# Kernel tuning notes

Hardware: AMD Instinct MI355X
Metric: run time of the kernel (lower is better)

The kernel has to match this reference:

```python
import jax, jax.numpy as jnp
import numpy as np

H, DH, DIM, BNECK, NK, COND = 8, 64, 256, 128, 32, 256


def _ln(x):
    m = x.mean(-1, keepdims=True)
    v = ((x - m) ** 2).mean(-1, keepdims=True)
    return (x - m) * jax.lax.rsqrt(v + 1e-5)


def _mlp(x, w1, b1, w2, b2):
    return jax.nn.gelu(x @ w1 + b1) @ w2 + b2


def _radial(d, w):
    # Bessel-type radial basis sin(n*d)/d projected to heads; limit n as d->0
    n = jnp.arange(1, NK + 1, dtype=d.dtype)
    safe = jnp.maximum(d, 1e-6)[..., None]
    basis = jnp.where(d[..., None] > 1e-6, jnp.sin(d[..., None] * n) / safe, n)
    return jnp.einsum('ijk,kh->hij', basis, w)


def _kernel(x, qk_w):
    # DotProductKernel with softmax=False, scale=1.0
    b, n, _ = x.shape
    qk = (x @ qk_w).reshape(b, n, 2, H, DH).transpose(0, 3, 2, 1, 4)  # b h two n d
    q, k = qk[:, :, 0], qk[:, :, 1]
    return jnp.einsum('bhid,bhjd->bhij', q, k)


def reference(u, lat, lat_diff, lon_diff, scalar_cond, adaLN_w, adaLN_b, to_v_w, to_x_in_w, to_x_w1, to_x_b1, to_x_w2, to_x_b2, to_y_in_w, to_y_w1, to_y_b1, to_y_w2, to_y_b2, kx_qk_w, ky_qk_w, rx_w, ry_w, merge_w, merge_b, ffn_w1, ffn_b1, ffn_w2, ffn_b2):
    b, nlat, nlon, c = u.shape
    mod = (scalar_cond @ adaLN_w + adaLN_b)[:, None, None]  # (b,1,1,6c)
    sh_msa, sc_msa, g_msa, sh_mlp, sc_mlp, g_mlp = jnp.split(mod, 6, axis=-1)
    u_skip = u
    um = _ln(u) * (1 + sc_msa) + sh_msa  # modulate_fused
    lw = jnp.cos(lat)
    lw = lw / lw.mean()
    # PoolingReducer over lat (weighted) -> (b, nlon, bneck)
    u_x = _mlp(jnp.einsum('bilc,cd,i->bld', um, to_x_in_w, lw) / nlat,
               to_x_w1, to_x_b1, to_x_w2, to_x_b2)
    # PoolingReducer over lon -> (b, nlat, bneck)
    u_y = _mlp((um @ to_y_in_w).mean(axis=2), to_y_w1, to_y_b1, to_y_w2, to_y_b2)
    k_x = jax.nn.softmax(_kernel(u_x, kx_qk_w) * _radial(lon_diff, rx_w)[None], axis=-1)
    k_y = jax.nn.softmax(_kernel(u_y, ky_qk_w) * _radial(lat_diff, ry_w)[None], axis=-1)
    v = (um @ to_v_w).reshape(b, nlat, nlon, H, DH).transpose(0, 3, 1, 2, 4)  # b h i l c
    u_phi = jnp.einsum('bhij,bhjmc->bhimc', k_y, v)
    u_phi = jnp.einsum('bhlm,bhimc->bhilc', k_x, u_phi)
    u_phi = u_phi.transpose(0, 2, 3, 1, 4)  # b i l h c
    mu = u_phi.mean(-1, keepdims=True)
    var = ((u_phi - mu) ** 2).mean(-1, keepdims=True)
    gn = ((u_phi - mu) * jax.lax.rsqrt(var + 1e-6)).reshape(b, nlat, nlon, H * DH)
    u1 = u_skip + g_msa * (gn @ merge_w + merge_b)  # bias_dropout_add_scale (inference)
    u2 = _ln(u1) * (1 + sc_mlp) + sh_mlp
    return u1 + g_mlp * _mlp(u2, ffn_w1, ffn_b1, ffn_w2, ffn_b2)


def setup_inputs():
    key = jax.random.key(0)
    ks = jax.random.split(key, 20)
    b, nlat, nlon = 4, 128, 256
    dim, h, dh, bn, cond = DIM, H, DH, BNECK, COND
    f = jnp.float32
    u = jax.random.normal(ks[0], (b, nlat, nlon, dim), f)
    lat = jnp.linspace(-np.pi / 2 + 0.01, np.pi / 2 - 0.01, nlat).astype(f)
    lat_diff = jnp.abs(lat[:, None] - lat[None, :])
    lon = (jnp.arange(nlon) * (2 * np.pi / nlon)).astype(f)
    d = jnp.abs(lon[:, None] - lon[None, :])
    lon_diff = jnp.minimum(d, 2 * np.pi - d)
    scalar_cond = jax.random.normal(ks[1], (b, cond), f)

    def w(k, shape, s=0.02):
        return jax.random.normal(k, shape, f) * s

    return dict(
        u=u, lat=lat, lat_diff=lat_diff, lon_diff=lon_diff, scalar_cond=scalar_cond,
        adaLN_w=w(ks[2], (cond, 6 * dim)), adaLN_b=w(ks[3], (6 * dim,)),
        to_v_w=w(ks[4], (dim, h * dh)),
        to_x_in_w=w(ks[5], (dim, dim)), to_x_w1=w(ks[6], (dim, dim)), to_x_b1=jnp.zeros((dim,), f),
        to_x_w2=w(ks[7], (dim, bn)), to_x_b2=jnp.zeros((bn,), f),
        to_y_in_w=w(ks[8], (dim, dim)), to_y_w1=w(ks[9], (dim, dim)), to_y_b1=jnp.zeros((dim,), f),
        to_y_w2=w(ks[10], (dim, bn)), to_y_b2=jnp.zeros((bn,), f),
        kx_qk_w=w(ks[11], (bn, 2 * h * dh)), ky_qk_w=w(ks[12], (bn, 2 * h * dh)),
        rx_w=w(ks[13], (NK, h), 0.1), ry_w=w(ks[14], (NK, h), 0.1),
        merge_w=w(ks[15], (h * dh, dim)), merge_b=jnp.zeros((dim,), f),
        ffn_w1=w(ks[16], (dim, 4 * dim)), ffn_b1=jnp.zeros((4 * dim,), f),
        ffn_w2=w(ks[17], (4 * dim, dim)), ffn_b2=jnp.zeros((dim,), f))
```

## Files before the change

kernel.cpp:

```cpp
#include <hip/hip_runtime.h>
#include <hip/hip_bf16.h>
#include <math.h>


#define B_ 4
#define NLAT 128
#define NLON 256
#define NTOK (B_*NLAT*NLON)
#define SLOT_ELE ((size_t)16777216)

typedef __hip_bfloat16 bf16;
typedef unsigned short u16;
typedef __attribute__((ext_vector_type(8))) short short8;
typedef __attribute__((ext_vector_type(4))) float f32x4;

__device__ __forceinline__ float b2f(bf16 x){ return __bfloat162float(x); }
__device__ __forceinline__ bf16  f2b(float x){ return __float2bfloat16(x); }
__device__ __forceinline__ u16 f2bits(float x){
  bf16 h = __float2bfloat16(x); return *(u16*)&h;
}
__device__ __forceinline__ float bits2f(u16 u){
  union { unsigned int i; float f; } v; v.i = ((unsigned int)u) << 16; return v.f;
}
__device__ __forceinline__ float gelu_f(float x){
  float x3 = x*x*x;
  return 0.5f*x*(1.0f + tanhf(0.7978845608028654f*(x + 0.044715f*x3)));
}
__device__ __forceinline__ float gelu_fast(float x){
  float t = 0.7978845608028654f*(x + 0.044715f*x*x*x);
  float e = __builtin_amdgcn_exp2f(t * 2.8853900817779268f);
  return x - x*__builtin_amdgcn_rcpf(e + 1.0f);
}
__device__ __forceinline__ float ldin(const void* p, size_t i, int flag){
  return flag ? b2f(((const bf16*)p)[i]) : ((const float*)p)[i];
}
__device__ __forceinline__ short4 pack4(float a, float b, float c, float d){
  short4 r; r.x = (short)f2bits(a); r.y = (short)f2bits(b);
  r.z = (short)f2bits(c); r.w = (short)f2bits(d); return r;
}
__device__ __forceinline__ short8 pack8(float a, float b, float c, float d,
                                        float e, float f, float g, float h){
  short8 r;
  r[0]=(short)f2bits(a); r[1]=(short)f2bits(b); r[2]=(short)f2bits(c); r[3]=(short)f2bits(d);
  r[4]=(short)f2bits(e); r[5]=(short)f2bits(f); r[6]=(short)f2bits(g); r[7]=(short)f2bits(h);
  return r;
}
__device__ __forceinline__ void stage16(const u16* g, u16* l){
  __builtin_amdgcn_global_load_lds(
      (const __attribute__((address_space(1))) void*)g,
      (__attribute__((address_space(3))) void*)l, 16, 0, 0);
}

__global__ void k_detect(const void* lon_diff, int* flag){
  const float c = 0.02454369260617026f;
  float asF = ((const float*)lon_diff)[1];
  float asB = b2f(((const bf16*)lon_diff)[1]);
  float ef = fabsf(asF - c), eb = fabsf(asB - c);
  if (!isfinite(ef)) ef = 1e30f;
  *flag = (eb < ef) ? 1 : 0;
}

struct CvtTab {
  const void* src[27];
  float* dst[27];
  int cum[28];
};
__global__ __launch_bounds__(256) void k_cvtall(CvtTab t, const int* __restrict__ flag,
                                                int total){
  int f = *flag;
  for (int i = blockIdx.x*256 + threadIdx.x; i < total; i += gridDim.x*256){
    int s = 0;
    while (i >= t.cum[s+1]) ++s;
    int off = i - t.cum[s];
    t.dst[s][off] = ldin(t.src[s], off, f);
  }
}

__global__ __launch_bounds__(256) void k_wprep(const float* __restrict__ W,
                                               u16* __restrict__ wf,
                                               int KS, int ldn, int total){
  int gid = blockIdx.x*256 + threadIdx.x;
  if (gid >= total) return;
  int j = gid & 7; int lane = (gid >> 3) & 63; int rest = gid >> 9;
  int ks = rest % KS; int nt = rest / KS;
  int k = ks*32 + (lane >> 4)*8 + j;
  int n = nt*16 + (lane & 15);
  wf[gid] = f2bits(W[(size_t)k*ldn + n]);
}

__global__ __launch_bounds__(256) void k_wprep2(const float* __restrict__ W,
                                                u16* __restrict__ wf){
  int gid = blockIdx.x*256 + threadIdx.x;
  int j = gid & 7; int lane = (gid >> 3) & 63; int rest = gid >> 9;
  int nt = rest & 15; int ksAll = rest >> 4;
  int k = ksAll*32 + (lane >> 4)*8 + j;
  int n = nt*16 + (lane & 15);
  wf[gid] = f2bits(W[(size_t)k*256 + n]);
}

__global__ __launch_bounds__(256) void k_wtrans(const float* __restrict__ W,
                                                u16* __restrict__ WT, int K, int N){
  int gid = blockIdx.x*256 + threadIdx.x;
  if (gid >= K*N) return;
  int k = gid % K, n = gid / K;
  WT[(size_t)n*K + k] = f2bits(W[(size_t)k*N + n]);
}

__global__ __launch_bounds__(256) void k_mod(const float* __restrict__ sc,
                                             const float* __restrict__ w,
                                             const float* __restrict__ bias,
                                             float* __restrict__ mod){
  int gid = blockIdx.x*256 + threadIdx.x;
  int s = gid / 1536, j = gid % 1536;
  float acc = bias[j];
  for (int c = 0; c < 256; ++c) acc += sc[s*256+c] * w[c*1536+j];
  mod[gid] = acc;
}

__global__ __launch_bounds__(128) void k_lw(const float* __restrict__ lat,
                                            float* __restrict__ lw){
  __shared__ float red[128];
  int i = threadIdx.x;
  float cv = cosf(lat[i]);
  red[i] = cv; __syncthreads();
  for (int s = 64; s > 0; s >>= 1){ if (i < s) red[i] += red[i+s]; __syncthreads(); }
  float mean = red[0] * (1.0f/128.0f);
  lw[i] = cv / mean;
}

__global__ __launch_bounds__(256) void k_um2(const void* __restrict__ u,
                                             const float* __restrict__ mod,
                                             u16* __restrict__ um,
                                             const int* __restrict__ flag){
  __shared__ u16 tile[64][264];
  __shared__ float r1[64][4], r2[64][4], mv[64], rs[64];
  __shared__ float ssh[256], ssc[256];
  int f = *flag; int tid = threadIdx.x;
  int t0 = blockIdx.x*64; int b = t0 >> 15;
  ssh[tid] = mod[b*1536 + tid];
  ssc[tid] = mod[b*1536 + 256 + tid];
  for (int it = 0; it < 16; ++it){
    int idx = it*256 + tid;
    int tok = idx >> 6, c4 = idx & 63;
    short4 v4;
    if (f){
      v4 = *(const short4*)((const bf16*)u + ((size_t)(t0+tok))*256 + c4*4);
    } else {
      float4 fv = ((const float4*)u)[((size_t)(t0+tok))*64 + c4];
      v4 = pack4(fv.x, fv.y, fv.z, fv.w);
    }
    *(short4*)&tile[tok][c4*4] = v4;
  }
  __syncthreads();
  {
    int tok = tid >> 2, part = tid & 3;
    float s1 = 0.f, s2 = 0.f;
    for (int c4 = 0; c4 < 16; ++c4){
      short4 v4 = *(const short4*)&tile[tok][part*64 + c4*4];
      float a = bits2f((u16)v4.x), bb = bits2f((u16)v4.y),
            c = bits2f((u16)v4.z), d = bits2f((u16)v4.w);
      s1 += a+bb+c+d; s2 += a*a+bb*bb+c*c+d*d;
    }
    r1[tok][part] = s1; r2[tok][part] = s2;
  }
  __syncthreads();
  if ((tid & 3) == 0){
    int tok = tid >> 2;
    float a1 = r1[tok][0]+r1[tok][1]+r1[tok][2]+r1[tok][3];
    float a2 = r2[tok][0]+r2[tok][1]+r2[tok][2]+r2[tok][3];
    float mean = a1*(1.0f/256.0f);
    float var = a2*(1.0f/256.0f) - mean*mean;
    mv[tok] = mean; rs[tok] = rsqrtf(var + 1e-5f);
  }
  __syncthreads();
  for (int it = 0; it < 16; ++it){
    int idx = it*256 + tid;
    int tok = idx >> 6, c4 = idx & 63;
    float mean = mv[tok], rstd = rs[tok];
    short4 v4 = *(const short4*)&tile[tok][c4*4];
    float y[4]; u16 raw[4] = {(u16)v4.x,(u16)v4.y,(u16)v4.z,(u16)v4.w};
    #pragma unroll
    for (int p = 0; p < 4; ++p){
      int c = c4*4 + p;
      y[p] = (bits2f(raw[p]) - mean)*rstd*(1.0f + ssc[c]) + ssh[c];
    }
    *(short4*)(um + ((size_t)(t0+tok))*256 + c4*4) = pack4(y[0],y[1],y[2],y[3]);
  }
}

__global__ __launch_bounds__(256) void k_redx(const u16* __restrict__ um,
                                              const float* __restrict__ lw,
                                              float* __restrict__ redx){
  __shared__ float lws[128];
  int tid = threadIdx.x;
  if (tid < 128) lws[tid] = lw[tid];
  __syncthreads();
  int gid = blockIdx.x*256 + tid;
  int c = gid & 255; int l = (gid >> 8) & 255; int b = gid >> 16;
  float acc = 0.0f;
  for (int i = 0; i < 128; ++i)
    acc += bits2f(um[(((size_t)(b*128 + i)*256 + l)*256) + c]) * lws[i];
  redx[gid] = acc * (1.0f/128.0f);
}

__global__ __launch_bounds__(256) void k_redy(const u16* __restrict__ um,
                                              float* __restrict__ redy){
  int gid = blockIdx.x*256 + threadIdx.x;
  int c = gid & 255; int i = (gid >> 8) & 127; int b = gid >> 15;
  float acc = 0.0f;
  for (int l = 0; l < 256; ++l)
    acc += bits2f(um[(((size_t)(b*128 + i)*256 + l)*256) + c]);
  redy[gid] = acc * (1.0f/256.0f);
}

__global__ __launch_bounds__(256) void gemm_row2(
    const float* __restrict__ Ax, const float* __restrict__ Wx,
    const float* __restrict__ bx, float* __restrict__ Cx, int Kx, int Nx,
    const float* __restrict__ Ay, const float* __restrict__ Wy,
    const float* __restrict__ by, float* __restrict__ Cy, int Ky, int Ny,
    int nbx, int act){
  __shared__ float As[256];
  int bid = blockIdx.x; int tid = threadIdx.x;
  const float* A; const float* W; const float* bias; float* C; int K, N, r;
  if (bid < nbx){ A=Ax; W=Wx; bias=bx; C=Cx; K=Kx; N=Nx; r=bid; }
  else          { A=Ay; W=Wy; bias=by; C=Cy; K=Ky; N=Ny; r=bid-nbx; }
  for (int k = tid; k < K; k += 256) As[k] = A[(size_t)r*K + k];
  __syncthreads();
  for (int n = tid; n < N; n += 256){
    float a0=0.f, a1=0.f, a2=0.f, a3=0.f;
    for (int k = 0; k < K; k += 4){
      a0 += As[k+0]*W[(size_t)(k+0)*N + n];
      a1 += As[k+1]*W[(size_t)(k+1)*N + n];
      a2 += As[k+2]*W[(size_t)(k+2)*N + n];
      a3 += As[k+3]*W[(size_t)(k+3)*N + n];
    }
    float acc = (a0+a1)+(a2+a3) + (bias ? bias[n] : 0.0f);
    if (act == 1) acc = gelu_f(acc);
    C[(size_t)r*N + n] = acc;
  }
}

__global__ __launch_bounds__(256) void k_radial(const float* __restrict__ d,
                                                const float* __restrict__ w,
                                                float* __restrict__ rad, int n){
  int gid = blockIdx.x*256 + threadIdx.x;
  int nn = n*n;
  int h = gid / nn; int rem = gid % nn;
  float dv = d[rem];
  float safe = fmaxf(dv, 1e-6f);
  float acc = 0.0f;
  for (int k = 0; k < 32; ++k){
    float nk = (float)(k+1);
    float basis = (dv > 1e-6f) ? (sinf(dv*nk)/safe) : nk;
    acc += basis * w[k*8 + h];
  }
  rad[gid] = acc;
}

__global__ __launch_bounds__(256) void k_qkT(const float* __restrict__ qk,
                                             float* __restrict__ kT, int n){
  int gid = blockIdx.x*256 + threadIdx.x;
  int j = gid % n; int rest = gid / n;
  int d = rest & 63; int bh = rest >> 6;
  int b = bh >> 3, h = bh & 7;
  kT[gid] = qk[((size_t)(b*n + j))*1024 + 512 + h*64 + d];
}

__global__ __launch_bounds__(256) void k_attn2(const float* __restrict__ qk,
                                               const float* __restrict__ kT,
                                               const float* __restrict__ rad,
                                               u16* __restrict__ kout, int n){
  extern __shared__ float sm[];
  float* qs = sm; float* red = sm + 64;
  int j = threadIdx.x;
  int bid = blockIdx.x; int i = bid % n; int h = (bid / n) & 7; int b = bid / (n*8);
  if (j < 64) qs[j] = qk[((size_t)(b*n + i))*1024 + h*64 + j];
  __syncthreads();
  const float* kcol = kT + ((size_t)((b*8 + h)*64))*n + j;
  float dot = 0.0f;
  #pragma unroll 8
  for (int d0 = 0; d0 < 64; ++d0) dot += qs[d0]*kcol[(size_t)d0*n];
  float s = dot * rad[((size_t)(h*n + i))*n + j];
  float m = s;
  #pragma unroll
  for (int off = 32; off; off >>= 1) m = fmaxf(m, __shfl_xor(m, off));
  int wv = j >> 6, nw = n >> 6;
  if ((j & 63) == 0) red[wv] = m;
  __syncthreads();
  m = red[0];
  for (int w = 1; w < nw; ++w) m = fmaxf(m, red[w]);
  float e = __builtin_amdgcn_exp2f((s - m)*1.44269504088896f);
  float t = e;
  #pragma unroll
  for (int off = 32; off; off >>= 1) t += __shfl_xor(t, off);
  if ((j & 63) == 0) red[4 + wv] = t;
  __syncthreads();
  t = 0.0f;
  for (int w = 0; w < nw; ++w) t += red[4 + w];
  kout[(size_t)bid*n + j] = f2bits(e / t);
}

__global__ __launch_bounds__(256, 2) void k_v3(const u16* __restrict__ um,
                                               const u16* __restrict__ WvT,
                                               u16* __restrict__ vA,
                                               int b0, size_t bstr){
  __shared__ __align__(16) u16 T[512][72];
  int tid = threadIdx.x;
  int wave = tid>>6, lane = tid&63, quad = lane>>4, l15 = lane&15;
  int bid = blockIdx.x;
  int b = b0 + (bid >> 9);
  int rem = bid & 511;
  int m = rem & 255, jt = rem >> 8;
  const u16* umb = um + ((size_t)b*32768)*256;
  f32x4 acc[8][4];
  #pragma unroll
  for (int mt = 0; mt < 8; ++mt)
    #pragma unroll
    for (int nt = 0; nt < 4; ++nt) acc[mt][nt] = (f32x4){0.f,0.f,0.f,0.f};
  for (int ks = 0; ks < 8; ++ks){
    short8 bfr[4];
    #pragma unroll
    for (int nt = 0; nt < 4; ++nt){
      int j = jt*64 + nt*16 + l15;
      bfr[nt] = *(const short8*)(umb + ((size_t)j*256 + m)*256 + ks*32 + quad*8);
    }
    #pragma unroll
    for (int mt = 0; mt < 8; ++mt){
      short8 a = *(const short8*)(WvT + (size_t)((wave*8+mt)*16 + l15)*256 + ks*32 + quad*8);
      #pragma unroll
      for (int nt = 0; nt < 4; ++nt)
        acc[mt][nt] = __builtin_amdgcn_mfma_f32_16x16x32_bf16(a, bfr[nt], acc[mt][nt], 0, 0, 0);
    }
  }
  #pragma unroll
  for (int mt = 0; mt < 8; ++mt){
    int hc0 = (wave*8+mt)*16 + quad*4;
    #pragma unroll
    for (int nt = 0; nt < 4; ++nt){
      int jp = nt*16 + l15;
      T[hc0+0][jp] = f2bits(acc[mt][nt][0]);
      T[hc0+1][jp] = f2bits(acc[mt][nt][1]);
      T[hc0+2][jp] = f2bits(acc[mt][nt][2]);
      T[hc0+3][jp] = f2bits(acc[mt][nt][3]);
    }
  }
  __syncthreads();
  u16* vAb = vA + (size_t)(b - b0)*bstr;
  for (int it = 0; it < 16; ++it){
    int idx = it*256 + tid;
    int g = idx & 7, hc = idx >> 3;
    short8 v8 = *(const short8*)&T[hc][g*8];
    int h = hc >> 6, c = hc & 63;
    *(short8*)(vAb + (size_t)h*2097152 + ((size_t)c*256 + m)*128 + jt*64 + g*8) = v8;
  }
}

__global__ __launch_bounds__(256) void k_phi1c(const u16* __restrict__ kyb,
                                               const u16* __restrict__ vA,
                                               u16* __restrict__ phi,
                                               int b0, size_t bstr){
  int tid = threadIdx.x;
  int wave = tid>>6, lane = tid&63, quad = lane>>4, l15 = lane&15;
  int bid = blockIdx.x;
  int b = b0 + (bid >> 9);
  int rem = bid & 511; int mblk = rem & 63, h = rem >> 6;
  int m0 = mblk*256;
  const u16* vAh = vA + (size_t)(b - b0)*bstr + (size_t)h*2097152;
  u16* phib = phi + (size_t)(b - b0)*bstr;
  const u16* kyh = kyb + (size_t)(b*8+h)*16384;
  f32x4 acc[4][8];
  #pragma unroll
  for (int mt = 0; mt < 4; ++mt)
    #pragma unroll
    for (int nt = 0; nt < 8; ++nt) acc[mt][nt] = (f32x4){0.f,0.f,0.f,0.f};
  for (int ks = 0; ks < 4; ++ks){
    short8 bfr[8];
    #pragma unroll
    for (int nt = 0; nt < 8; ++nt)
      bfr[nt] = *(const short8*)(kyh + (size_t)(nt*16 + l15)*128 + ks*32 + quad*8);
    #pragma unroll
    for (int mt = 0; mt < 4; ++mt){
      int cm = m0 + (wave*4+mt)*16 + l15;
      short8 a = *(const short8*)(vAh + (size_t)cm*128 + ks*32 + quad*8);
      #pragma unroll
      for (int nt = 0; nt < 8; ++nt)
        acc[mt][nt] = __builtin_amdgcn_mfma_f32_16x16x32_bf16(a, bfr[nt], acc[mt][nt], 0, 0, 0);
    }
  }
  #pragma unroll
  for (int mt = 0; mt < 4; ++mt){
    int cmr = m0 + (wave*4+mt)*16 + quad*4;
    #pragma unroll
    for (int nt = 0; nt < 8; ++nt){
      int i = nt*16 + l15;
      *(short4*)(phib + (size_t)h*2097152 + (size_t)i*16384 + cmr)
        = pack4(acc[mt][nt][0], acc[mt][nt][1], acc[mt][nt][2], acc[mt][nt][3]);
    }
  }
}

__global__ __launch_bounds__(256) void k_phi2b(const u16* __restrict__ kxb,
                                               const u16* __restrict__ phi,
                                               u16* __restrict__ OUTt,
                                               int b0, size_t bstr){
  int tid = threadIdx.x;
  int wave = tid>>6, lane = tid&63, quad = lane>>4, l15 = lane&15;
  int bid = blockIdx.x;
  int b = b0 + (bid >> 9);
  int rem = bid & 511; int mblk = rem & 63, h = rem >> 6;
  int m0 = mblk*128;
  int mhalf = (wave&1)*4, nhalf = (wave>>1)*8;
  const u16* ph = phi + (size_t)(b - b0)*bstr + (size_t)h*2097152;
  u16* OUTb = OUTt + (size_t)(b - b0)*bstr;
  const u16* kxh = kxb + (size_t)(b*8+h)*65536;
  f32x4 acc[4][8];
  #pragma unroll
  for (int mt = 0; mt < 4; ++mt)
    #pragma unroll
    for (int nt = 0; nt < 8; ++nt) acc[mt][nt] = (f32x4){0.f,0.f,0.f,0.f};
  for (int ks = 0; ks < 8; ++ks){
    short8 bfr[8];
    #pragma unroll
    for (int nt = 0; nt < 8; ++nt)
      bfr[nt] = *(const short8*)(kxh + (size_t)((nhalf+nt)*16 + l15)*256 + ks*32 + quad*8);
    #pragma unroll
    for (int mt = 0; mt < 4; ++mt){
      int m2 = m0 + (mhalf+mt)*16 + l15;
      short8 a = *(const short8*)(ph + (size_t)m2*256 + ks*32 + quad*8);
      #pragma unroll
      for (int nt = 0; nt < 8; ++nt)
        acc[mt][nt] = __builtin_amdgcn_mfma_f32_16x16x32_bf16(a, bfr[nt], acc[mt][nt], 0, 0, 0);
    }
  }
  #pragma unroll
  for (int mt = 0; mt < 4; ++mt){
    int m2r = m0 + (mhalf+mt)*16 + quad*4;
    #pragma unroll
    for (int nt = 0; nt < 8; ++nt){
      int l = (nhalf+nt)*16 + l15;
      *(short4*)(OUTb + (size_t)h*2097152 + (size_t)l*8192 + m2r)
        = pack4(acc[mt][nt][0], acc[mt][nt][1], acc[mt][nt][2], acc[mt][nt][3]);
    }
  }
}

__global__ __launch_bounds__(256) void k_gnb(const u16* __restrict__ OUTt,
                                             u16* __restrict__ gn,
                                             int b0, size_t bstr){
  int tid = threadIdx.x;
  int bid = blockIdx.x;
  int bi = bid >> 11;
  int rem = bid & 2047; int l = rem & 255, h = rem >> 8;
  int i = tid >> 1, half = tid & 1;
  const u16* src = OUTt + (size_t)bi*bstr + (size_t)h*2097152 + (size_t)l*8192 + i*64 + half*32;
  float v[32]; float s1 = 0.f, s2 = 0.f;
  #pragma unroll
  for (int c4 = 0; c4 < 8; ++c4){
    short4 v4 = *(const short4*)(src + c4*4);
    v[c4*4+0] = bits2f((u16)v4.x); v[c4*4+1] = bits2f((u16)v4.y);
    v[c4*4+2] = bits2f((u16)v4.z); v[c4*4+3] = bits2f((u16)v4.w);
  }
  #pragma unroll
  for (int c = 0; c < 32; ++c){ s1 += v[c]; s2 += v[c]*v[c]; }
  s1 += __shfl_xor(s1, 1); s2 += __shfl_xor(s2, 1);
  float mean = s1*(1.0f/64.0f);
  float var = s2*(1.0f/64.0f) - mean*mean;
  float rstd = rsqrtf(var + 1e-6f);
  u16* dst = gn + (size_t)bi*bstr + ((size_t)(i*256 + l))*512 + h*64 + half*32;
  #pragma unroll
  for (int c4 = 0; c4 < 8; ++c4)
    *(short4*)(dst + c4*4) = pack4((v[c4*4+0]-mean)*rstd, (v[c4*4+1]-mean)*rstd,
                                   (v[c4*4+2]-mean)*rstd, (v[c4*4+3]-mean)*rstd);
}

__global__ __launch_bounds__(256) void k_mergeb(const u16* __restrict__ gn,
                                                const u16* __restrict__ WmT,
                                                const float* __restrict__ biasm,
                                                const float* __restrict__ mod,
                                                const void* __restrict__ u,
                                                void* __restrict__ outv,
                                                const int* __restrict__ flag,
                                                int b0, size_t bstr){
  __shared__ float smg[256], sbb[256];
  int f = *flag;
  int tid = threadIdx.x;
  int bid = blockIdx.x;
  int b = b0 + (bid >> 8);
  int t0 = (bid & 255)*128;
  smg[tid] = mod[b*1536 + 512 + tid];
  sbb[tid] = biasm[tid];
  __syncthreads();
  int wave = tid>>6, lane = tid&63, quad = lane>>4, l15 = lane&15;
  const u16* gnb = gn + (size_t)(b - b0)*bstr;
  int nt0 = wave*2;
  f32x4 acc[16][2];
  #pragma unroll
  for (int mt = 0; mt < 16; ++mt){ acc[mt][0] = (f32x4){0.f,0.f,0.f,0.f}; acc[mt][1] = (f32x4){0.f,0.f,0.f,0.f}; }
  for (int ks = 0; ks < 16; ++ks){
    short8 bfr[2];
    #pragma unroll
    for (int nti = 0; nti < 2; ++nti){
      int tok = t0 + (nt0+nti)*16 + l15;
      bfr[nti] = *(const short8*)(gnb + (size_t)tok*512 + ks*32 + quad*8);
    }
    #pragma unroll
    for (int mt = 0; mt < 16; ++mt){
      short8 a = *(const short8*)(WmT + (size_t)(mt*16 + l15)*512 + ks*32 + quad*8);
      #pragma unroll
      for (int nti = 0; nti < 2; ++nti)
        acc[mt][nti] = __builtin_amdgcn_mfma_f32_16x16x32_bf16(a, bfr[nti], acc[mt][nti], 0, 0, 0);
    }
  }
  #pragma unroll
  for (int mt = 0; mt < 16; ++mt){
    int d0 = mt*16 + quad*4;
    #pragma unroll
    for (int nti = 0; nti < 2; ++nti){
      int tok = t0 + (nt0+nti)*16 + l15;
      size_t o = ((size_t)b*32768 + tok)*256 + d0;
      float r0,r1,r2,r3;
      if (f){
        short4 rv = *(const short4*)((const bf16*)u + o);
        r0 = bits2f((u16)rv.x); r1 = bits2f((u16)rv.y); r2 = bits2f((u16)rv.z); r3 = bits2f((u16)rv.w);
      } else {
        float4 rv = *(const float4*)((const float*)u + o);
        r0 = rv.x; r1 = rv.y; r2 = rv.z; r3 = rv.w;
      }
      float y0 = r0 + smg[d0+0]*(acc[mt][nti][0] + sbb[d0+0]);
      float y1 = r1 + smg[d0+1]*(acc[mt][nti][1] + sbb[d0+1]);
      float y2 = r2 + smg[d0+2]*(acc[mt][nti][2] + sbb[d0+2]);
      float y3 = r3 + smg[d0+3]*(acc[mt][nti][3] + sbb[d0+3]);
      if (f) *(short4*)((bf16*)outv + o) = pack4(y0,y1,y2,y3);
      else   *(float4*)((float*)outv + o) = (float4){y0,y1,y2,y3};
    }
  }
}

__global__ __launch_bounds__(256, 2) void k_ffn4(
    const float* __restrict__ mod,
    const u16* __restrict__ w1f,
    const float* __restrict__ b1c,
    const u16* __restrict__ w2f,
    const float* __restrict__ b2c,
    void* __restrict__ outv,
    const int* __restrict__ flag){
  __shared__ __align__(16) u16 wbuf[2][16384];
  __shared__ __align__(16) u16 hs[64][40];
  int f = *flag;
  int tid = threadIdx.x;
  int wave = tid>>6, lane = tid&63, quad = lane>>4, l15 = lane&15;
  int mrow = wave*16;
  int t0 = blockIdx.x*64;
  int bb = t0 >> 15;
  const float* modp = mod + bb*1536;
  size_t rowbase = ((size_t)(t0 + mrow + l15))*256;

  {
    #pragma unroll
    for (int i = 0; i < 8; ++i){
      int seg = wave*8 + i;
      const u16* src = (seg < 16)
          ? (w1f + (size_t)seg*512 + lane*8)
          : (w2f + (size_t)(seg-16)*512 + lane*8);
      stage16(src, &wbuf[0][seg*512]);
    }
  }

  short8 afr[8];
  float s1 = 0.f, s2 = 0.f;
  #pragma unroll
  for (int ks = 0; ks < 8; ++ks){
    int c0 = ks*32 + quad*8;
    float v0,v1,v2,v3,v4,v5,v6,v7;
    if (f){
      short8 r = *(const short8*)((const bf16*)outv + rowbase + c0);
      afr[ks] = r;
      v0 = bits2f((u16)r[0]); v1 = bits2f((u16)r[1]); v2 = bits2f((u16)r[2]); v3 = bits2f((u16)r[3]);
      v4 = bits2f((u16)r[4]); v5 = bits2f((u16)r[5]); v6 = bits2f((u16)r[6]); v7 = bits2f((u16)r[7]);
    } else {
      float4 fa = *(const float4*)((const float*)outv + rowbase + c0);
      float4 fb = *(const float4*)((const float*)outv + rowbase + c0 + 4);
      v0=fa.x; v1=fa.y; v2=fa.z; v3=fa.w; v4=fb.x; v5=fb.y; v6=fb.z; v7=fb.w;
      afr[ks] = pack8(v0,v1,v2,v3,v4,v5,v6,v7);
    }
    s1 += v0+v1+v2+v3+v4+v5+v6+v7;
    s2 += v0*v0+v1*v1+v2*v2+v3*v3+v4*v4+v5*v5+v6*v6+v7*v7;
  }
  s1 += __shfl_xor(s1, 16); s1 += __shfl_xor(s1, 32);
  s2 += __shfl_xor(s2, 16); s2 += __shfl_xor(s2, 32);
  float mean = s1*(1.0f/256.0f);
  float var = s2*(1.0f/256.0f) - mean*mean;
  float rstd = rsqrtf(var + 1e-5f);
  #pragma unroll
  for (int ks = 0; ks < 8; ++ks){
    int c0 = ks*32 + quad*8;
    float4 sh0 = *(const float4*)&modp[768 + c0];
    float4 sh1 = *(const float4*)&modp[768 + c0 + 4];
    float4 sc0 = *(const float4*)&modp[1024 + c0];
    float4 sc1 = *(const float4*)&modp[1024 + c0 + 4];
    short8 r = afr[ks];
    float y0 = (bits2f((u16)r[0]) - mean)*rstd*(1.0f+sc0.x) + sh0.x;
    float y1 = (bits2f((u16)r[1]) - mean)*rstd*(1.0f+sc0.y) + sh0.y;
    float y2 = (bits2f((u16)r[2]) - mean)*rstd*(1.0f+sc0.z) + sh0.z;
    float y3 = (bits2f((u16)r[3]) - mean)*rstd*(1.0f+sc0.w) + sh0.w;
    float y4 = (bits2f((u16)r[4]) - mean)*rstd*(1.0f+sc1.x) + sh1.x;
    float y5 = (bits2f((u16)r[5]) - mean)*rstd*(1.0f+sc1.y) + sh1.y;
    float y6 = (bits2f((u16)r[6]) - mean)*rstd*(1.0f+sc1.z) + sh1.z;
    float y7 = (bits2f((u16)r[7]) - mean)*rstd*(1.0f+sc1.w) + sh1.w;
    afr[ks] = pack8(y0,y1,y2,y3,y4,y5,y6,y7);
  }

  __syncthreads();

  f32x4 acc2[16];
  #pragma unroll
  for (int nt = 0; nt < 16; ++nt) acc2[nt] = (f32x4){0.f,0.f,0.f,0.f};
  int buf = 0;
  #pragma unroll 1
  for (int c = 0; c < 32; ++c){
    if (c < 31){
      int cn = c + 1;
      #pragma unroll
      for (int i = 0; i < 8; ++i){
        int seg = wave*8 + i;
        const u16* src = (seg < 16)
            ? (w1f + (size_t)cn*8192 + (size_t)seg*512 + lane*8)
            : (w2f + (size_t)cn*8192 + (size_t)(seg-16)*512 + lane*8);
        stage16(src, &wbuf[buf^1][seg*512]);
      }
    }
    const u16* w1l = &wbuf[buf][0];
    const u16* w2l = &wbuf[buf][8192];
    f32x4 acc1[2];
    acc1[0] = (f32x4){0.f,0.f,0.f,0.f}; acc1[1] = (f32x4){0.f,0.f,0.f,0.f};
    #pragma unroll
    for (int ks = 0; ks < 8; ++ks){
      #pragma unroll
      for (int nt2 = 0; nt2 < 2; ++nt2){
        short8 bfr = *(const short8*)(w1l + (nt2*8 + ks)*512 + lane*8);
        acc1[nt2] = __builtin_amdgcn_mfma_f32_16x16x32_bf16(afr[ks], bfr, acc1[nt2], 0, 0, 0);
      }
    }
    __builtin_amdgcn_sched_barrier(0);
    #pragma unroll
    for (int nt2 = 0; nt2 < 2; ++nt2){
      int hid = nt2*16 + l15;
      float b1 = b1c[c*32 + hid];
      #pragma unroll
      for (int r = 0; r < 4; ++r)
        hs[mrow + quad*4 + r][hid] = f2bits(gelu_fast(acc1[nt2][r] + b1));
    }
    __builtin_amdgcn_sched_barrier(0);
    asm volatile("s_waitcnt lgkmcnt(0)" ::: "memory");
    __builtin_amdgcn_sched_barrier(0);
    short8 a2 = *(const short8*)&hs[mrow + l15][quad*8];
    #pragma unroll
    for (int nt = 0; nt < 16; ++nt){
      short8 bfr = *(const short8*)(w2l + nt*512 + lane*8);
      acc2[nt] = __builtin_amdgcn_mfma_f32_16x16x32_bf16(a2, bfr, acc2[nt], 0, 0, 0);
    }
    __syncthreads();
    buf ^= 1;
  }

  #pragma unroll
  for (int nt = 0; nt < 16; ++nt){
    int col = nt*16 + l15;
    float g = modp[1280 + col];
    float b2v = b2c[col];
    #pragma unroll
    for (int r = 0; r < 4; ++r){
      size_t o = ((size_t)(t0 + mrow + quad*4 + r))*256 + col;
      float resid = f ? bits2f(((const u16*)outv)[o]) : ((const float*)outv)[o];
      float y = resid + g*(acc2[nt][r] + b2v);
      if (f) ((u16*)outv)[o] = f2bits(y);
      else   ((float*)outv)[o] = y;
    }
  }
}

extern "C" void kernel_launch(void* const* d_in, const int* in_sizes, int n_in,
                              void* d_out, int out_size, void* d_ws, size_t ws_size,
                              hipStream_t stream){
  (void)n_in; (void)out_size;

  char* p = (char*)d_ws;
  auto alloc = [&](size_t bytes)->void*{
    void* r = (void*)p; p += (bytes + 255) & ~(size_t)255; return r;
  };

  int* flag = (int*)alloc(4);
  float* cin[28];
  cin[0] = nullptr;
  for (int i = 1; i < 28; ++i) cin[i] = (float*)alloc((size_t)in_sizes[i]*4);

  float* mod  = (float*)alloc((size_t)4*1536*4);
  float* lw   = (float*)alloc((size_t)128*4);
  float* redx = (float*)alloc((size_t)4*256*256*4);
  float* redy = (float*)alloc((size_t)4*128*256*4);
  float* tx   = (float*)alloc((size_t)4*256*256*4);
  float* hx   = (float*)alloc((size_t)4*256*256*4);
  float* uxb  = (float*)alloc((size_t)4*256*128*4);
  float* ty   = (float*)alloc((size_t)4*128*256*4);
  float* hy   = (float*)alloc((size_t)4*128*256*4);
  float* uyb  = (float*)alloc((size_t)4*128*128*4);
  float* qkx  = (float*)alloc((size_t)4*256*1024*4);
  float* qky  = (float*)alloc((size_t)4*128*1024*4);
  float* kTx  = (float*)alloc((size_t)4*8*64*256*4);
  float* kTy  = (float*)alloc((size_t)4*8*64*128*4);
  float* radx = (float*)alloc((size_t)8*256*256*4);
  float* rady = (float*)alloc((size_t)8*128*128*4);
  u16* kxb = (u16*)alloc((size_t)32*256*256*2);
  u16* kyb = (u16*)alloc((size_t)32*128*128*2);
  u16* w1f = (u16*)alloc((size_t)256*1024*2);
  u16* w2f = (u16*)alloc((size_t)1024*256*2);
  u16* WvT = (u16*)alloc((size_t)512*256*2);
  u16* WmT = (u16*)alloc((size_t)256*512*2);
  u16* um  = (u16*)alloc((size_t)NTOK*256*2);

  size_t used = (size_t)(p - (char*)d_ws);
  int merged = (ws_size > used) && ((ws_size - used) >= (size_t)8*SLOT_ELE*2 + 65536);
  size_t slotBytes = (merged ? 4 : 1) * SLOT_ELE * 2;
  u16* slotV = (u16*)alloc(slotBytes);
  u16* slotP = (u16*)alloc(slotBytes);

  const void* u = d_in[0];

  k_detect<<<1, 1, 0, stream>>>(d_in[3], flag);
  {
    CvtTab t;
    int cum = 0;
    for (int i = 1; i < 28; ++i){
      t.src[i-1] = d_in[i];
      t.dst[i-1] = cin[i];
      t.cum[i-1] = cum;
      cum += in_sizes[i];
    }
    t.cum[27] = cum;
    k_cvtall<<<2048, 256, 0, stream>>>(t, flag, cum);
  }
  k_wprep<<<1024, 256, 0, stream>>>(cin[24], w1f, 8, 1024, 256*1024);
  k_wprep2<<<1024, 256, 0, stream>>>(cin[26], w2f);
  k_wtrans<<<512, 256, 0, stream>>>(cin[7],  WvT, 256, 512);
  k_wtrans<<<512, 256, 0, stream>>>(cin[22], WmT, 512, 256);

  k_mod<<<24, 256, 0, stream>>>(cin[4], cin[5], cin[6], mod);
  k_lw<<<1, 128, 0, stream>>>(cin[1], lw);
  k_um2<<<NTOK/64, 256, 0, stream>>>(u, mod, um, flag);
  k_redx<<<1024, 256, 0, stream>>>(um, lw, redx);
  k_redy<<<512, 256, 0, stream>>>(um, redy);
  gemm_row2<<<1536, 256, 0, stream>>>(redx, cin[8],  nullptr,  tx,  256, 256,
                                      redy, cin[13], nullptr,  ty,  256, 256, 1024, 0);
  gemm_row2<<<1536, 256, 0, stream>>>(tx,   cin[9],  cin[10],  hx,  256, 256,
                                      ty,   cin[14], cin[15],  hy,  256, 256, 1024, 1);
  gemm_row2<<<1536, 256, 0, stream>>>(hx,   cin[11], cin[12],  uxb, 256, 128,
                                      hy,   cin[16], cin[17],  uyb, 256, 128, 1024, 0);
  gemm_row2<<<1536, 256, 0, stream>>>(uxb,  cin[18], nullptr,  qkx, 128, 1024,
                                      uyb,  cin[19], nullptr,  qky, 128, 1024, 1024, 0);
  k_radial<<<(8*256*256)/256, 256, 0, stream>>>(cin[3], cin[20], radx, 256);
  k_radial<<<(8*128*128)/256, 256, 0, stream>>>(cin[2], cin[21], rady, 128);
  k_qkT<<<2048, 256, 0, stream>>>(qkx, kTx, 256);
  k_qkT<<<1024, 256, 0, stream>>>(qky, kTy, 128);
  k_attn2<<<4*8*256, 256, (64+8)*4, stream>>>(qkx, kTx, radx, kxb, 256);
  k_attn2<<<4*8*128, 128, (64+8)*4, stream>>>(qky, kTy, rady, kyb, 128);

  if (merged){
    k_v3    <<<2048, 256, 0, stream>>>(um, WvT, slotV, 0, SLOT_ELE);
    k_phi1c <<<2048, 256, 0, stream>>>(kyb, slotV, slotP, 0, SLOT_ELE);
    k_phi2b <<<2048, 256, 0, stream>>>(kxb, slotP, slotV, 0, SLOT_ELE);
    k_gnb   <<<8192, 256, 0, stream>>>(slotV, slotP, 0, SLOT_ELE);
    k_mergeb<<<1024, 256, 0, stream>>>(slotP, WmT, cin[23], mod, u, d_out, flag, 0, SLOT_ELE);
  } else {
    for (int b = 0; b < 4; ++b){
      k_v3    <<<512, 256, 0, stream>>>(um, WvT, slotV, b, 0);
      k_phi1c <<<512, 256, 0, stream>>>(kyb, slotV, slotP, b, 0);
      k_phi2b <<<512, 256, 0, stream>>>(kxb, slotP, slotV, b, 0);
      k_gnb   <<<2048, 256, 0, stream>>>(slotV, slotP, b, 0);
      k_mergeb<<<256, 256, 0, stream>>>(slotP, WmT, cin[23], mod, u, d_out, flag, b, 0);
    }
  }
  k_ffn4<<<NTOK/64, 256, 0, stream>>>(mod, w1f, cin[25], w2f, cin[27], d_out, flag);
}
```

Measured before the change: 1.452 ms.

## Double FFN row tile per block and transpose K through shared-memory tiles

The fused FFN kernel now handles 128 tokens per block (32 rows per wave) instead of 64. Each weight chunk staged into shared memory now feeds twice as many MFMAs, which halves weight traffic per token and the number of blocks. The cost is double the accumulator and A-fragment registers under launch_bounds(256,2), which risks spills or lower occupancy. Separately, the K transpose now goes through a padded 64x64 shared-memory tile so both its reads and writes are coalesced, replacing strided gathers.

```diff
diff --git a/kernel.cpp b/kernel.cpp
--- a/kernel.cpp
+++ b/kernel.cpp
@@ -257,13 +257,25 @@
   rad[gid] = acc;
 }
 
-__global__ __launch_bounds__(256) void k_qkT(const float* __restrict__ qk,
-                                             float* __restrict__ kT, int n){
-  int gid = blockIdx.x*256 + threadIdx.x;
-  int j = gid % n; int rest = gid / n;
-  int d = rest & 63; int bh = rest >> 6;
-  int b = bh >> 3, h = bh & 7;
-  kT[gid] = qk[((size_t)(b*n + j))*1024 + 512 + h*64 + d];
+__global__ __launch_bounds__(256) void k_qkT2(const float* __restrict__ qk,
+                                              float* __restrict__ kT, int n){
+  __shared__ float tile[64][65];
+  int tid = threadIdx.x;
+  int bid = blockIdx.x;
+  int ntj = n >> 6;
+  int jt = bid % ntj; int h = (bid / ntj) & 7; int b = bid / (ntj*8);
+  int j0 = jt*64;
+  for (int it = 0; it < 16; ++it){
+    int idx = it*256 + tid;
+    int jr = idx >> 6, d = idx & 63;
+    tile[jr][d] = qk[((size_t)(b*n + j0 + jr))*1024 + 512 + h*64 + d];
+  }
+  __syncthreads();
+  for (int it = 0; it < 16; ++it){
+    int idx = it*256 + tid;
+    int dr = idx >> 6, j = idx & 63;
+    kT[((size_t)((b*8 + h)*64 + dr))*n + j0 + j] = tile[j][dr];
+  }
 }
 
 __global__ __launch_bounds__(256) void k_attn2(const float* __restrict__ qk,
@@ -536,7 +548,7 @@
   }
 }
 
-__global__ __launch_bounds__(256, 2) void k_ffn4(
+__global__ __launch_bounds__(256, 2) void k_ffn5(
     const float* __restrict__ mod,
     const u16* __restrict__ w1f,
     const float* __restrict__ b1c,
@@ -545,15 +557,14 @@
     void* __restrict__ outv,
     const int* __restrict__ flag){
   __shared__ __align__(16) u16 wbuf[2][16384];
-  __shared__ __align__(16) u16 hs[64][40];
+  __shared__ __align__(16) u16 hs[128][40];
   int f = *flag;
   int tid = threadIdx.x;
   int wave = tid>>6, lane = tid&63, quad = lane>>4, l15 = lane&15;
-  int mrow = wave*16;
-  int t0 = blockIdx.x*64;
+  int mrow = wave*32;
+  int t0 = blockIdx.x*128;
   int bb = t0 >> 15;
   const float* modp = mod + bb*1536;
-  size_t rowbase = ((size_t)(t0 + mrow + l15))*256;
 
   {
     #pragma unroll
@@ -566,55 +577,61 @@
     }
   }
 
-  short8 afr[8];
-  float s1 = 0.f, s2 = 0.f;
-  #pragma unroll
-  for (int ks = 0; ks < 8; ++ks){
-    int c0 = ks*32 + quad*8;
-    float v0,v1,v2,v3,v4,v5,v6,v7;
-    if (f){
-      short8 r = *(const short8*)((const bf16*)outv + rowbase + c0);
-      afr[ks] = r;
-      v0 = bits2f((u16)r[0]); v1 = bits2f((u16)r[1]); v2 = bits2f((u16)r[2]); v3 = bits2f((u16)r[3]);
-      v4 = bits2f((u16)r[4]); v5 = bits2f((u16)r[5]); v6 = bits2f((u16)r[6]); v7 = bits2f((u16)r[7]);
-    } else {
-      float4 fa = *(const float4*)((const float*)outv + rowbase + c0);
-      float4 fb = *(const float4*)((const float*)outv + rowbase + c0 + 4);
-      v0=fa.x; v1=fa.y; v2=fa.z; v3=fa.w; v4=fb.x; v5=fb.y; v6=fb.z; v7=fb.w;
-      afr[ks] = pack8(v0,v1,v2,v3,v4,v5,v6,v7);
-    }
-    s1 += v0+v1+v2+v3+v4+v5+v6+v7;
-    s2 += v0*v0+v1*v1+v2*v2+v3*v3+v4*v4+v5*v5+v6*v6+v7*v7;
-  }
-  s1 += __shfl_xor(s1, 16); s1 += __shfl_xor(s1, 32);
-  s2 += __shfl_xor(s2, 16); s2 += __shfl_xor(s2, 32);
-  float mean = s1*(1.0f/256.0f);
-  float var = s2*(1.0f/256.0f) - mean*mean;
-  float rstd = rsqrtf(var + 1e-5f);
-  #pragma unroll
-  for (int ks = 0; ks < 8; ++ks){
-    int c0 = ks*32 + quad*8;
-    float4 sh0 = *(const float4*)&modp[768 + c0];
-    float4 sh1 = *(const float4*)&modp[768 + c0 + 4];
-    float4 sc0 = *(const float4*)&modp[1024 + c0];
-    float4 sc1 = *(const float4*)&modp[1024 + c0 + 4];
-    short8 r = afr[ks];
-    float y0 = (bits2f((u16)r[0]) - mean)*rstd*(1.0f+sc0.x) + sh0.x;
-    float y1 = (bits2f((u16)r[1]) - mean)*rstd*(1.0f+sc0.y) + sh0.y;
-    float y2 = (bits2f((u16)r[2]) - mean)*rstd*(1.0f+sc0.z) + sh0.z;
-    float y3 = (bits2f((u16)r[3]) - mean)*rstd*(1.0f+sc0.w) + sh0.w;
-    float y4 = (bits2f((u16)r[4]) - mean)*rstd*(1.0f+sc1.x) + sh1.x;
-    float y5 = (bits2f((u16)r[5]) - mean)*rstd*(1.0f+sc1.y) + sh1.y;
-    float y6 = (bits2f((u16)r[6]) - mean)*rstd*(1.0f+sc1.z) + sh1.z;
-    float y7 = (bits2f((u16)r[7]) - mean)*rstd*(1.0f+sc1.w) + sh1.w;
-    afr[ks] = pack8(y0,y1,y2,y3,y4,y5,y6,y7);
-  }
-
-  __syncthreads();
-
-  f32x4 acc2[16];
-  #pragma unroll
-  for (int nt = 0; nt < 16; ++nt) acc2[nt] = (f32x4){0.f,0.f,0.f,0.f};
+  short8 afr[2][8];
+  #pragma unroll
+  for (int s = 0; s < 2; ++s){
+    size_t rowbase = ((size_t)(t0 + mrow + s*16 + l15))*256;
+    float s1 = 0.f, s2 = 0.f;
+    #pragma unroll
+    for (int ks = 0; ks < 8; ++ks){
+      int c0 = ks*32 + quad*8;
+      float v0,v1,v2,v3,v4,v5,v6,v7;
+      if (f){
+        short8 r = *(const short8*)((const bf16*)outv + rowbase + c0);
+        afr[s][ks] = r;
+        v0 = bits2f((u16)r[0]); v1 = bits2f((u16)r[1]); v2 = bits2f((u16)r[2]); v3 = bits2f((u16)r[3]);
+        v4 = bits2f((u16)r[4]); v5 = bits2f((u16)r[5]); v6 = bits2f((u16)r[6]); v7 = bits2f((u16)r[7]);
+      } else {
+        float4 fa = *(const float4*)((const float*)outv + rowbase + c0);
+        float4 fb = *(const float4*)((const float*)outv + rowbase + c0 + 4);
+        v0=fa.x; v1=fa.y; v2=fa.z; v3=fa.w; v4=fb.x; v5=fb.y; v6=fb.z; v7=fb.w;
+        afr[s][ks] = pack8(v0,v1,v2,v3,v4,v5,v6,v7);
+      }
+      s1 += v0+v1+v2+v3+v4+v5+v6+v7;
+      s2 += v0*v0+v1*v1+v2*v2+v3*v3+v4*v4+v5*v5+v6*v6+v7*v7;
+    }
+    s1 += __shfl_xor(s1, 16); s1 += __shfl_xor(s1, 32);
+    s2 += __shfl_xor(s2, 16); s2 += __shfl_xor(s2, 32);
+    float mean = s1*(1.0f/256.0f);
+    float var = s2*(1.0f/256.0f) - mean*mean;
+    float rstd = rsqrtf(var + 1e-5f);
+    #pragma unroll
+    for (int ks = 0; ks < 8; ++ks){
+      int c0 = ks*32 + quad*8;
+      float4 sh0 = *(const float4*)&modp[768 + c0];
+      float4 sh1 = *(const float4*)&modp[768 + c0 + 4];
+      float4 sc0 = *(const float4*)&modp[1024 + c0];
+      float4 sc1 = *(const float4*)&modp[1024 + c0 + 4];
+      short8 r = afr[s][ks];
+      float y0 = (bits2f((u16)r[0]) - mean)*rstd*(1.0f+sc0.x) + sh0.x;
+      float y1 = (bits2f((u16)r[1]) - mean)*rstd*(1.0f+sc0.y) + sh0.y;
+      float y2 = (bits2f((u16)r[2]) - mean)*rstd*(1.0f+sc0.z) + sh0.z;
+      float y3 = (bits2f((u16)r[3]) - mean)*rstd*(1.0f+sc0.w) + sh0.w;
+      float y4 = (bits2f((u16)r[4]) - mean)*rstd*(1.0f+sc1.x) + sh1.x;
+      float y5 = (bits2f((u16)r[5]) - mean)*rstd*(1.0f+sc1.y) + sh1.y;
+      float y6 = (bits2f((u16)r[6]) - mean)*rstd*(1.0f+sc1.z) + sh1.z;
+      float y7 = (bits2f((u16)r[7]) - mean)*rstd*(1.0f+sc1.w) + sh1.w;
+      afr[s][ks] = pack8(y0,y1,y2,y3,y4,y5,y6,y7);
+    }
+  }
+
+  __syncthreads();
+
+  f32x4 acc2[2][16];
+  #pragma unroll
+  for (int s = 0; s < 2; ++s)
+    #pragma unroll
+    for (int nt = 0; nt < 16; ++nt) acc2[s][nt] = (f32x4){0.f,0.f,0.f,0.f};
   int buf = 0;
   #pragma unroll 1
   for (int c = 0; c < 32; ++c){
@@ -631,14 +648,16 @@
     }
     const u16* w1l = &wbuf[buf][0];
     const u16* w2l = &wbuf[buf][8192];
-    f32x4 acc1[2];
-    acc1[0] = (f32x4){0.f,0.f,0.f,0.f}; acc1[1] = (f32x4){0.f,0.f,0.f,0.f};
+    f32x4 acc1[2][2];
+    acc1[0][0] = (f32x4){0.f,0.f,0.f,0.f}; acc1[0][1] = (f32x4){0.f,0.f,0.f,0.f};
+    acc1[1][0] = (f32x4){0.f,0.f,0.f,0.f}; acc1[1][1] = (f32x4){0.f,0.f,0.f,0.f};
     #pragma unroll
     for (int ks = 0; ks < 8; ++ks){
       #pragma unroll
       for (int nt2 = 0; nt2 < 2; ++nt2){
         short8 bfr = *(const short8*)(w1l + (nt2*8 + ks)*512 + lane*8);
-        acc1[nt2] = __builtin_amdgcn_mfma_f32_16x16x32_bf16(afr[ks], bfr, acc1[nt2], 0, 0, 0);
+        acc1[0][nt2] = __builtin_amdgcn_mfma_f32_16x16x32_bf16(afr[0][ks], bfr, acc1[0][nt2], 0, 0, 0);
+        acc1[1][nt2] = __builtin_amdgcn_mfma_f32_16x16x32_bf16(afr[1][ks], bfr, acc1[1][nt2], 0, 0, 0);
       }
     }
     __builtin_amdgcn_sched_barrier(0);
@@ -647,17 +666,21 @@
       int hid = nt2*16 + l15;
       float b1 = b1c[c*32 + hid];
       #pragma unroll
-      for (int r = 0; r < 4; ++r)
-        hs[mrow + quad*4 + r][hid] = f2bits(gelu_fast(acc1[nt2][r] + b1));
+      for (int s = 0; s < 2; ++s)
+        #pragma unroll
+        for (int r = 0; r < 4; ++r)
+          hs[mrow + s*16 + quad*4 + r][hid] = f2bits(gelu_fast(acc1[s][nt2][r] + b1));
     }
     __builtin_amdgcn_sched_barrier(0);
     asm volatile("s_waitcnt lgkmcnt(0)" ::: "memory");
     __builtin_amdgcn_sched_barrier(0);
-    short8 a2 = *(const short8*)&hs[mrow + l15][quad*8];
+    short8 a2_0 = *(const short8*)&hs[mrow + l15][quad*8];
+    short8 a2_1 = *(const short8*)&hs[mrow + 16 + l15][quad*8];
     #pragma unroll
     for (int nt = 0; nt < 16; ++nt){
       short8 bfr = *(const short8*)(w2l + nt*512 + lane*8);
-      acc2[nt] = __builtin_amdgcn_mfma_f32_16x16x32_bf16(a2, bfr, acc2[nt], 0, 0, 0);
+      acc2[0][nt] = __builtin_amdgcn_mfma_f32_16x16x32_bf16(a2_0, bfr, acc2[0][nt], 0, 0, 0);
+      acc2[1][nt] = __builtin_amdgcn_mfma_f32_16x16x32_bf16(a2_1, bfr, acc2[1][nt], 0, 0, 0);
     }
     __syncthreads();
     buf ^= 1;
@@ -669,13 +692,15 @@
     float g = modp[1280 + col];
     float b2v = b2c[col];
     #pragma unroll
-    for (int r = 0; r < 4; ++r){
-      size_t o = ((size_t)(t0 + mrow + quad*4 + r))*256 + col;
-      float resid = f ? bits2f(((const u16*)outv)[o]) : ((const float*)outv)[o];
-      float y = resid + g*(acc2[nt][r] + b2v);
-      if (f) ((u16*)outv)[o] = f2bits(y);
-      else   ((float*)outv)[o] = y;
-    }
+    for (int s = 0; s < 2; ++s)
+      #pragma unroll
+      for (int r = 0; r < 4; ++r){
+        size_t o = ((size_t)(t0 + mrow + s*16 + quad*4 + r))*256 + col;
+        float resid = f ? bits2f(((const u16*)outv)[o]) : ((const float*)outv)[o];
+        float y = resid + g*(acc2[s][nt][r] + b2v);
+        if (f) ((u16*)outv)[o] = f2bits(y);
+        else   ((float*)outv)[o] = y;
+      }
   }
 }
 
@@ -759,8 +784,8 @@
                                       uyb,  cin[19], nullptr,  qky, 128, 1024, 1024, 0);
   k_radial<<<(8*256*256)/256, 256, 0, stream>>>(cin[3], cin[20], radx, 256);
   k_radial<<<(8*128*128)/256, 256, 0, stream>>>(cin[2], cin[21], rady, 128);
-  k_qkT<<<2048, 256, 0, stream>>>(qkx, kTx, 256);
-  k_qkT<<<1024, 256, 0, stream>>>(qky, kTy, 128);
+  k_qkT2<<<4*8*4, 256, 0, stream>>>(qkx, kTx, 256);
+  k_qkT2<<<4*8*2, 256, 0, stream>>>(qky, kTy, 128);
   k_attn2<<<4*8*256, 256, (64+8)*4, stream>>>(qkx, kTx, radx, kxb, 256);
   k_attn2<<<4*8*128, 128, (64+8)*4, stream>>>(qky, kTy, rady, kyb, 128);
 
@@ -779,5 +804,5 @@
       k_mergeb<<<256, 256, 0, stream>>>(slotP, WmT, cin[23], mod, u, d_out, flag, b, 0);
     }
   }
-  k_ffn4<<<NTOK/64, 256, 0, stream>>>(mod, w1f, cin[25], w2f, cin[27], d_out, flag);
-}
+  k_ffn5<<<NTOK/128, 256, 0, stream>>>(mod, w1f, cin[25], w2f, cin[27], d_out, flag);
+}
```

Result: slower. 1.596 ms (+9.9%).
